# Optimization experiments

Measured on AMD Instinct MI355X. Metric: run time of the kernel, lower is better.

## Reference

```python
import jax, jax.numpy as jnp
import numpy as np

C = 1.0
TAU = 1.0
LE = 1.0
LH = 1.0
LN_EPS = 1e-5

def _safe_norm(x, keepdims=False):
    return jnp.clip(jnp.sqrt(jnp.sum(x * x, axis=-1, keepdims=keepdims)), 1e-15)

def _project_to_ball(x, c, eps=1e-5):
    sqrt_c = c ** 0.5
    norm = _safe_norm(x, keepdims=True)
    max_norm = (1.0 - eps) / sqrt_c
    scale = jnp.where(norm > max_norm, max_norm / norm, 1.0)
    return x * scale

def _lambda_x(x, c):
    x = _project_to_ball(x, c)
    x2 = jnp.sum(x * x, axis=-1, keepdims=True)
    return 2.0 / jnp.clip(1.0 - c * x2, 1e-15)

def _mobius_add(x, y, c):
    x = _project_to_ball(x, c)
    y = _project_to_ball(y, c)
    x2 = jnp.sum(x * x, axis=-1, keepdims=True)
    y2 = jnp.sum(y * y, axis=-1, keepdims=True)
    xy = jnp.sum(x * y, axis=-1, keepdims=True)
    num = (1 + 2 * c * xy + c * y2) * x + (1 - c * x2) * y
    den = 1 + 2 * c * xy + c ** 2 * x2 * y2
    return num / jnp.clip(den, 1e-15)

def _exp_map_x(x, v, c):
    sqrt_c = c ** 0.5
    lam = _lambda_x(x, c)
    vnorm = _safe_norm(v, keepdims=True)
    v_dir = v / vnorm
    factor = jnp.tanh(lam * sqrt_c * vnorm / 2.0) / sqrt_c
    out = _mobius_add(x, v_dir * factor, c)
    return _project_to_ball(out, c)

def _log_map_x(x, y, c):
    sqrt_c = c ** 0.5
    lam = _lambda_x(x, c)
    u = _mobius_add(-x, y, c)
    unorm = _safe_norm(u, keepdims=True)
    u_dir = u / unorm
    arg = jnp.minimum(sqrt_c * unorm, 1 - 1e-7)
    scale = 2.0 / (lam * sqrt_c) * jnp.arctanh(arg)
    return scale * u_dir

def _poincare_distance_sq(x, y, c):
    sqrt_c = c ** 0.5
    x = _project_to_ball(x, c)
    y = _project_to_ball(y, c)
    diff = _mobius_add(-x, y, c)
    norm = _safe_norm(diff, keepdims=False)
    arg = jnp.minimum(sqrt_c * norm, 1 - 1e-7)
    dist = 2.0 / sqrt_c * jnp.arctanh(arg)
    return dist * dist

def setup_inputs() -> dict:
    key = jax.random.key(0)
    ks = jax.random.split(key, 6)
    B, N, L, A, de, dh, z_dim = 8, 8, 64, 64, 128, 64, 128
    z_e, z_h = z_dim // 2 + z_dim % 2, z_dim // 2
    return {
        "curr_rho_batch": jax.random.normal(ks[0], (B, A, de), jnp.float32),
        "curr_hyp_emb": 0.1 * jax.random.normal(ks[1], (B, dh), jnp.float32),
        "demo_rho_batch": jax.random.normal(ks[2], (B, N, L, A, de), jnp.float32),
        "demo_hyp_emb": 0.1 * jax.random.normal(ks[3], (B, N, L, dh), jnp.float32),
        "We": 0.02 * jax.random.normal(ks[4], (z_e, de), jnp.float32),
        "Wh": 0.02 * jax.random.normal(ks[5], (z_h, dh), jnp.float32),
        "ln_gamma": jnp.ones((z_dim,), jnp.float32),
        "ln_beta": jnp.zeros((z_dim,), jnp.float32),
    }

def reference(curr_rho_batch, curr_hyp_emb, demo_rho_batch, demo_hyp_emb, We, Wh, ln_gamma, ln_beta):
    B, A, de = curr_rho_batch.shape
    _, N, L, _, _ = demo_rho_batch.shape
    M = N * L
    dh = curr_hyp_emb.shape[-1]
    demo_rho_flat = demo_rho_batch.reshape(B, M, A, de)   # [B,M,A,de]
    demo_hyp_flat = demo_hyp_emb.reshape(B, M, dh)        # [B,M,dh]
    # Euclidean squared distances: [B,M,A] -> [B,A,M]
    e_diff_sq = jnp.sum((curr_rho_batch[:, None, :, :] - demo_rho_flat) ** 2, axis=-1)
    e_diff_sq = jnp.transpose(e_diff_sq, (0, 2, 1))
    # Hyperbolic squared distances: [B,M]
    dH2 = _poincare_distance_sq(curr_hyp_emb[:, None, :], demo_hyp_flat, C)
    scores = -(LH * dH2[:, None, :] + LE * e_diff_sq) / max(TAU, 1e-8)  # [B,A,M]
    alpha = jax.nn.softmax(scores, axis=-1)
    # Euclidean aggregation
    e_out = jnp.einsum('bam,bmad->bad', alpha, demo_rho_flat)  # [B,A,de]
    # Hyperbolic Karcher-mean step
    log_vecs = _log_map_x(curr_hyp_emb[:, None, :], demo_hyp_flat, C)  # [B,M,dh]
    v = jnp.einsum('bam,bmd->bad', alpha, log_vecs)  # [B,A,dh]
    x_ba = jnp.broadcast_to(curr_hyp_emb[:, None, :], (B, A, dh))
    h_out = _exp_map_x(x_ba, v, C)  # [B,A,dh]
    z = jnp.concatenate([e_out @ We.T, h_out @ Wh.T], axis=-1)  # [B,A,z_dim]
    mean = jnp.mean(z, axis=-1, keepdims=True)
    var = jnp.var(z, axis=-1, keepdims=True)
    z = (z - mean) / jnp.sqrt(var + LN_EPS) * ln_gamma + ln_beta
    return z
```

## Files before the change

### kernel.cpp

```cpp
#include <hip/hip_runtime.h>

#define DEV __device__ __forceinline__

constexpr int A_ = 64, DE = 128, M_ = 512, DH = 64;

DEV float wred_sum64(float v) {
#pragma unroll
    for (int o = 1; o < 64; o <<= 1) v += __shfl_xor(v, o, 64);
    return v;
}

__global__ __launch_bounds__(256) void k_hyp(const float* __restrict__ curr_hyp,
                                             const float* __restrict__ demo_hyp,
                                             float* __restrict__ dH2,
                                             float* __restrict__ logv) {
    const int lane = threadIdx.x & 63;
    const int r    = (blockIdx.x << 2) + (threadIdx.x >> 6);
    const int b    = r >> 9;

    float x = curr_hyp[(b << 6) + lane];
    float y = demo_hyp[((size_t)r << 6) + lane];
    const float mx = 1.0f - 1e-5f;

    float x2r = wred_sum64(x * x);
    float xn  = fmaxf(sqrtf(x2r), 1e-15f);
    float sx  = xn > mx ? mx / xn : 1.0f;
    x *= sx;
    float x2 = x2r * sx * sx;
    float y2r = wred_sum64(y * y);
    float yn  = fmaxf(sqrtf(y2r), 1e-15f);
    float sy  = yn > mx ? mx / yn : 1.0f;
    y *= sy;
    float y2 = y2r * sy * sy;

    float xy = wred_sum64(x * y);
    float num = (1.f - 2.f * xy + y2) * (-x) + (1.f - x2) * y;
    float den = fmaxf(1.f - 2.f * xy + x2 * y2, 1e-15f);
    float u   = num / den;

    float u2  = wred_sum64(u * u);
    float un  = fmaxf(sqrtf(u2), 1e-15f);
    float arg = fminf(un, 1.f - 1e-7f);
    float at  = 0.5f * __logf((1.f + arg) / (1.f - arg));

    if (lane == 0) dH2[r] = 4.f * at * at;

    float lamden = fmaxf(1.f - x2, 1e-15f);
    float ls     = lamden * at / un;
    logv[((size_t)r << 6) + lane] = ls * u;
}

__global__ __launch_bounds__(512, 4) void k_main(const float* __restrict__ curr_rho,
                                                 const float* __restrict__ demo_rho,
                                                 const float* __restrict__ curr_hyp,
                                                 const float* __restrict__ dH2,
                                                 const float* __restrict__ logv,
                                                 const float* __restrict__ We,
                                                 const float* __restrict__ Wh,
                                                 const float* __restrict__ gamma,
                                                 const float* __restrict__ beta,
                                                 float* __restrict__ out) {
    __shared__ __align__(16) float buf[2][32 * 132];
    __shared__ float lds_sc[512];
    __shared__ float lds_dh[512];
    __shared__ float redmax[8];
    __shared__ float redsum[8];
    __shared__ float vpart[8][64];
    __shared__ float eh[192];

    const int t    = threadIdx.x;
    const int lane = t & 63;
    const int wv   = t >> 6;
    const int dp   = t & 15;
    const int mi   = t >> 4;
    const int blk  = blockIdx.x;
    const int b    = blk >> 6, a = blk & 63;

    lds_dh[t] = dH2[(b << 9) + t];

    float qf[8];
    {
        float4 q0 = *(const float4*)(curr_rho + (size_t)blk * DE + dp * 8);
        float4 q1 = *(const float4*)(curr_rho + (size_t)blk * DE + dp * 8 + 4);
        qf[0] = q0.x; qf[1] = q0.y; qf[2] = q0.z; qf[3] = q0.w;
        qf[4] = q1.x; qf[5] = q1.y; qf[6] = q1.z; qf[7] = q1.w;
    }

    const size_t rowStride = (size_t)A_ * DE;
    const float* base_ba = demo_rho + ((size_t)b * M_ * A_ + a) * DE;
    const int r0 = t >> 5, part = t & 31;

    {
        float4 s0 = *(const float4*)(base_ba + (size_t)r0 * rowStride + part * 4);
        float4 s1 = *(const float4*)(base_ba + (size_t)(r0 + 16) * rowStride + part * 4);
        *(float4*)&buf[0][r0 * 132 + part * 4]        = s0;
        *(float4*)&buf[0][(r0 + 16) * 132 + part * 4] = s1;
    }

    float e_acc[8];
#pragma unroll
    for (int j = 0; j < 8; j++) e_acc[j] = 0.f;
    float gmax = -1e30f, gsum = 0.f;

    for (int c = 0; c < 16; ++c) {
        const int cur = c & 1;
        float4 n0, n1;
        if (c < 15) {
            const float* dbase = base_ba + (size_t)(c + 1) * 32 * rowStride;
            n0 = *(const float4*)(dbase + (size_t)r0 * rowStride + part * 4);
            n1 = *(const float4*)(dbase + (size_t)(r0 + 16) * rowStride + part * 4);
        }
        __syncthreads();

        float kf[8];
        {
            float4 k0 = *(const float4*)&buf[cur][mi * 132 + dp * 8];
            float4 k1 = *(const float4*)&buf[cur][mi * 132 + dp * 8 + 4];
            kf[0] = k0.x; kf[1] = k0.y; kf[2] = k0.z; kf[3] = k0.w;
            kf[4] = k1.x; kf[5] = k1.y; kf[6] = k1.z; kf[7] = k1.w;
        }
        float ps = 0.f;
#pragma unroll
        for (int j = 0; j < 8; j++) { float d = qf[j] - kf[j]; ps += d * d; }
        ps += __shfl_xor(ps, 1, 64);
        ps += __shfl_xor(ps, 2, 64);
        ps += __shfl_xor(ps, 4, 64);
        ps += __shfl_xor(ps, 8, 64);
        float sc = -(lds_dh[c * 32 + mi] + ps);
        if (dp == 0) lds_sc[c * 32 + mi] = sc;

        float lm = fmaxf(sc, __shfl_xor(sc, 16, 64));
        lm = fmaxf(lm, __shfl_xor(lm, 32, 64));
        float wexp = __expf(sc - lm);
        float wsum = wexp + __shfl_xor(wexp, 16, 64);
        wsum += __shfl_xor(wsum, 32, 64);
        if (lane == 0) { redmax[wv] = lm; redsum[wv] = wsum; }
        __syncthreads();

        float cmax = redmax[0];
#pragma unroll
        for (int w = 1; w < 8; w++) cmax = fmaxf(cmax, redmax[w]);
        float csum = 0.f;
#pragma unroll
        for (int w = 0; w < 8; w++) csum += redsum[w] * __expf(redmax[w] - cmax);
        float gnew = fmaxf(gmax, cmax);
        float r1 = __expf(gmax - gnew);
        float r2 = __expf(cmax - gnew);
        gsum = gsum * r1 + csum * r2;
        float w = __expf(sc - gnew);
#pragma unroll
        for (int j = 0; j < 8; j++) e_acc[j] = fmaf(w, kf[j], e_acc[j] * r1);
        gmax = gnew;

        if (c < 15) {
            *(float4*)&buf[cur ^ 1][r0 * 132 + part * 4]        = n0;
            *(float4*)&buf[cur ^ 1][(r0 + 16) * 132 + part * 4] = n1;
        }
    }

    const float inv = 1.f / gsum;
    float al = __expf(lds_sc[t] - gmax) * inv;
    lds_sc[t] = al;

    float* rede = buf[0];
    *(float4*)&rede[mi * 132 + dp * 8]     = make_float4(e_acc[0], e_acc[1], e_acc[2], e_acc[3]);
    *(float4*)&rede[mi * 132 + dp * 8 + 4] = make_float4(e_acc[4], e_acc[5], e_acc[6], e_acc[7]);
    __syncthreads();
    if (t < 128) {
        float s = 0.f;
#pragma unroll
        for (int g = 0; g < 32; g++) s += rede[g * 132 + t];
        eh[t] = s * inv;
    }

    {
        const float* lvb = logv + ((size_t)(b * M_) + wv * 64) * DH;
        float acc = 0.f;
#pragma unroll 8
        for (int i = 0; i < 64; ++i)
            acc = fmaf(lds_sc[wv * 64 + i], lvb[(size_t)i * DH + lane], acc);
        vpart[wv][lane] = acc;
    }
    __syncthreads();

    if (wv == 0) {
        float v = 0.f;
#pragma unroll
        for (int w = 0; w < 8; w++) v += vpart[w][lane];

        const float mx = 1.0f - 1e-5f;
        float x = curr_hyp[(b << 6) + lane];
        float x2r = wred_sum64(x * x);
        float xn  = fmaxf(sqrtf(x2r), 1e-15f);
        float sx  = xn > mx ? mx / xn : 1.f;
        x *= sx;
        float x2 = x2r * sx * sx;
        float lamden = fmaxf(1.f - x2, 1e-15f);

        float v2 = wred_sum64(v * v);
        float vn = fmaxf(sqrtf(v2), 1e-15f);
        float targ   = vn / lamden;
        float e2     = __expf(2.f * targ);
        float factor = 1.f - 2.f / (e2 + 1.f);
        float wvv    = v * (factor / vn);

        float w2 = wred_sum64(wvv * wvv);
        float xw = wred_sum64(x * wvv);
        float num = (1.f + 2.f * xw + w2) * x + (1.f - x2) * wvv;
        float den = fmaxf(1.f + 2.f * xw + x2 * w2, 1e-15f);
        float h   = num / den;
        float h2  = wred_sum64(h * h);
        float hn  = fmaxf(sqrtf(h2), 1e-15f);
        float shh = hn > mx ? mx / hn : 1.f;
        h *= shh;
        eh[128 + lane] = h;

        float ze = 0.f;
        const float* werow = We + lane * 128;
#pragma unroll
        for (int d0 = 0; d0 < 128; d0 += 4) {
            float4 wv4 = *(const float4*)(werow + d0);
            ze = fmaf(eh[d0 + 0], wv4.x, ze);
            ze = fmaf(eh[d0 + 1], wv4.y, ze);
            ze = fmaf(eh[d0 + 2], wv4.z, ze);
            ze = fmaf(eh[d0 + 3], wv4.w, ze);
        }
        float zh = 0.f;
        const float* whrow = Wh + lane * 64;
#pragma unroll
        for (int d0 = 0; d0 < 64; d0 += 4) {
            float4 wv4 = *(const float4*)(whrow + d0);
            zh = fmaf(eh[128 + d0 + 0], wv4.x, zh);
            zh = fmaf(eh[128 + d0 + 1], wv4.y, zh);
            zh = fmaf(eh[128 + d0 + 2], wv4.z, zh);
            zh = fmaf(eh[128 + d0 + 3], wv4.w, zh);
        }
        float ssum = wred_sum64(ze + zh);
        float mean = ssum * (1.f / 128.f);
        float sq   = wred_sum64(ze * ze + zh * zh);
        float var  = sq * (1.f / 128.f) - mean * mean;
        float rinv = rsqrtf(var + 1e-5f);
        float oe = (ze - mean) * rinv * gamma[lane] + beta[lane];
        float oh = (zh - mean) * rinv * gamma[64 + lane] + beta[64 + lane];
        out[(size_t)blk * 128 + lane]      = oe;
        out[(size_t)blk * 128 + 64 + lane] = oh;
    }
}

extern "C" void kernel_launch(void* const* d_in, const int* in_sizes, int n_in,
                              void* d_out, int out_size, void* d_ws, size_t ws_size,
                              hipStream_t stream) {
    const float* curr_rho = (const float*)d_in[0];
    const float* curr_hyp = (const float*)d_in[1];
    const float* demo_rho = (const float*)d_in[2];
    const float* demo_hyp = (const float*)d_in[3];
    const float* We       = (const float*)d_in[4];
    const float* Wh       = (const float*)d_in[5];
    const float* gamma    = (const float*)d_in[6];
    const float* beta     = (const float*)d_in[7];
    float* out = (float*)d_out;

    float* ws   = (float*)d_ws;
    float* dH2  = ws;
    float* logv = ws + 4096;

    k_hyp<<<1024, 256, 0, stream>>>(curr_hyp, demo_hyp, dH2, logv);
    k_main<<<512, 512, 0, stream>>>(curr_rho, demo_rho, curr_hyp, dH2, logv,
                                    We, Wh, gamma, beta, out);
}
```

Before: 210.1 us.

## Use per-wave online softmax with register prefetch instead of LDS double buffering

Each wave now keeps its own running max and sum for the online softmax and merges the eight waves' partial states only once after the loop. This removes the two block-wide barriers per chunk. Demo rows are loaded straight into registers with a two-chunk-deep prefetch, replacing the shared-memory double buffer and its copy step. The trade-off is more live registers, and each thread loads its own 32-byte slice directly from global memory rather than through a cooperatively coalesced staging layout.

```diff
diff --git a/kernel.cpp b/kernel.cpp
--- a/kernel.cpp
+++ b/kernel.cpp
@@ -60,11 +60,11 @@
                                                  const float* __restrict__ gamma,
                                                  const float* __restrict__ beta,
                                                  float* __restrict__ out) {
-    __shared__ __align__(16) float buf[2][32 * 132];
+    __shared__ __align__(16) float rede[32 * 132];
     __shared__ float lds_sc[512];
     __shared__ float lds_dh[512];
-    __shared__ float redmax[8];
-    __shared__ float redsum[8];
+    __shared__ float redm[8];
+    __shared__ float reds[8];
     __shared__ float vpart[8][64];
     __shared__ float eh[192];
 
@@ -87,38 +87,33 @@
     }
 
     const size_t rowStride = (size_t)A_ * DE;
-    const float* base_ba = demo_rho + ((size_t)b * M_ * A_ + a) * DE;
-    const int r0 = t >> 5, part = t & 31;
-
-    {
-        float4 s0 = *(const float4*)(base_ba + (size_t)r0 * rowStride + part * 4);
-        float4 s1 = *(const float4*)(base_ba + (size_t)(r0 + 16) * rowStride + part * 4);
-        *(float4*)&buf[0][r0 * 132 + part * 4]        = s0;
-        *(float4*)&buf[0][(r0 + 16) * 132 + part * 4] = s1;
-    }
+    const size_t cstep     = (size_t)32 * rowStride;
+    const float* tp = demo_rho + ((size_t)b * M_ * A_ + a) * DE + (size_t)mi * rowStride + dp * 8;
+
+    __syncthreads();
+
+    float4 ka0 = *(const float4*)tp;
+    float4 ka1 = *(const float4*)(tp + 4);
+    float4 kb0 = *(const float4*)(tp + cstep);
+    float4 kb1 = *(const float4*)(tp + cstep + 4);
 
     float e_acc[8];
 #pragma unroll
     for (int j = 0; j < 8; j++) e_acc[j] = 0.f;
     float gmax = -1e30f, gsum = 0.f;
 
+#pragma unroll 2
     for (int c = 0; c < 16; ++c) {
-        const int cur = c & 1;
         float4 n0, n1;
-        if (c < 15) {
-            const float* dbase = base_ba + (size_t)(c + 1) * 32 * rowStride;
-            n0 = *(const float4*)(dbase + (size_t)r0 * rowStride + part * 4);
-            n1 = *(const float4*)(dbase + (size_t)(r0 + 16) * rowStride + part * 4);
+        if (c + 2 < 16) {
+            const float* np = tp + (size_t)(c + 2) * cstep;
+            n0 = *(const float4*)np;
+            n1 = *(const float4*)(np + 4);
         }
-        __syncthreads();
-
         float kf[8];
-        {
-            float4 k0 = *(const float4*)&buf[cur][mi * 132 + dp * 8];
-            float4 k1 = *(const float4*)&buf[cur][mi * 132 + dp * 8 + 4];
-            kf[0] = k0.x; kf[1] = k0.y; kf[2] = k0.z; kf[3] = k0.w;
-            kf[4] = k1.x; kf[5] = k1.y; kf[6] = k1.z; kf[7] = k1.w;
-        }
+        kf[0] = ka0.x; kf[1] = ka0.y; kf[2] = ka0.z; kf[3] = ka0.w;
+        kf[4] = ka1.x; kf[5] = ka1.y; kf[6] = ka1.z; kf[7] = ka1.w;
+
         float ps = 0.f;
 #pragma unroll
         for (int j = 0; j < 8; j++) { float d = qf[j] - kf[j]; ps += d * d; }
@@ -131,41 +126,40 @@
 
         float lm = fmaxf(sc, __shfl_xor(sc, 16, 64));
         lm = fmaxf(lm, __shfl_xor(lm, 32, 64));
-        float wexp = __expf(sc - lm);
+        float gnew = fmaxf(gmax, lm);
+        float r1   = __expf(gmax - gnew);
+        float wexp = __expf(sc - gnew);
         float wsum = wexp + __shfl_xor(wexp, 16, 64);
         wsum += __shfl_xor(wsum, 32, 64);
-        if (lane == 0) { redmax[wv] = lm; redsum[wv] = wsum; }
-        __syncthreads();
-
-        float cmax = redmax[0];
-#pragma unroll
-        for (int w = 1; w < 8; w++) cmax = fmaxf(cmax, redmax[w]);
-        float csum = 0.f;
-#pragma unroll
-        for (int w = 0; w < 8; w++) csum += redsum[w] * __expf(redmax[w] - cmax);
-        float gnew = fmaxf(gmax, cmax);
-        float r1 = __expf(gmax - gnew);
-        float r2 = __expf(cmax - gnew);
-        gsum = gsum * r1 + csum * r2;
-        float w = __expf(sc - gnew);
-#pragma unroll
-        for (int j = 0; j < 8; j++) e_acc[j] = fmaf(w, kf[j], e_acc[j] * r1);
+        gsum = fmaf(gsum, r1, wsum);
+#pragma unroll
+        for (int j = 0; j < 8; j++) e_acc[j] = fmaf(wexp, kf[j], e_acc[j] * r1);
         gmax = gnew;
 
-        if (c < 15) {
-            *(float4*)&buf[cur ^ 1][r0 * 132 + part * 4]        = n0;
-            *(float4*)&buf[cur ^ 1][(r0 + 16) * 132 + part * 4] = n1;
-        }
-    }
-
-    const float inv = 1.f / gsum;
-    float al = __expf(lds_sc[t] - gmax) * inv;
+        ka0 = kb0; ka1 = kb1; kb0 = n0; kb1 = n1;
+    }
+
+    if (lane == 0) { redm[wv] = gmax; reds[wv] = gsum; }
+    __syncthreads();
+
+    float M = redm[0];
+#pragma unroll
+    for (int w = 1; w < 8; w++) M = fmaxf(M, redm[w]);
+    float S = 0.f;
+#pragma unroll
+    for (int w = 0; w < 8; w++) S += reds[w] * __expf(redm[w] - M);
+    const float inv = 1.f / S;
+    const float fw  = __expf(gmax - M);
+
+    float al = __expf(lds_sc[t] - M) * inv;
+
+    *(float4*)&rede[mi * 132 + dp * 8] =
+        make_float4(e_acc[0] * fw, e_acc[1] * fw, e_acc[2] * fw, e_acc[3] * fw);
+    *(float4*)&rede[mi * 132 + dp * 8 + 4] =
+        make_float4(e_acc[4] * fw, e_acc[5] * fw, e_acc[6] * fw, e_acc[7] * fw);
     lds_sc[t] = al;
-
-    float* rede = buf[0];
-    *(float4*)&rede[mi * 132 + dp * 8]     = make_float4(e_acc[0], e_acc[1], e_acc[2], e_acc[3]);
-    *(float4*)&rede[mi * 132 + dp * 8 + 4] = make_float4(e_acc[4], e_acc[5], e_acc[6], e_acc[7]);
-    __syncthreads();
+    __syncthreads();
+
     if (t < 128) {
         float s = 0.f;
 #pragma unroll
```

Measured after the change: 209.9 us. Within noise of the previous version (-0.1%).
